# Optimization experiments

Measured on AMD Instinct MI355X. Metric: run time of the kernel, lower is better.

Reference implementation:

```python
import jax, jax.numpy as jnp
import numpy as np

EPS = 1e-12
B, S, H, NH = 4, 2048, 512, 8
DH = H // NH

def layernorm(x, g, b):
    mu = jnp.mean(x, axis=-1, keepdims=True)
    var = jnp.mean((x - mu) ** 2, axis=-1, keepdims=True)
    return (x - mu) * jax.lax.rsqrt(var + EPS) * g + b

def setup_inputs() -> dict:
    key = jax.random.key(0)
    ks = jax.random.split(key, 12)
    s = 0.02
    return {
        "hidden_states": jax.random.normal(ks[0], (B, S, H), dtype=jnp.float32),
        "attention_mask": jnp.zeros((B, 1, 1, S), dtype=jnp.float32),
        "ln1_g": jnp.ones((H,), jnp.float32), "ln1_b": jnp.zeros((H,), jnp.float32),
        "wq": jax.random.normal(ks[1], (H, H), jnp.float32) * s, "bq": jnp.zeros((H,), jnp.float32),
        "wk": jax.random.normal(ks[2], (H, H), jnp.float32) * s, "bk": jnp.zeros((H,), jnp.float32),
        "wv": jax.random.normal(ks[3], (H, H), jnp.float32) * s, "bv": jnp.zeros((H,), jnp.float32),
        "wo": jax.random.normal(ks[4], (H, H), jnp.float32) * s, "bo": jnp.zeros((H,), jnp.float32),
        "ln2_g": jnp.ones((H,), jnp.float32), "ln2_b": jnp.zeros((H,), jnp.float32),
    }

def _heads(x):  # [B,S,H] -> [B,NH,S,DH]
    return x.reshape(B, S, NH, DH).transpose(0, 2, 1, 3)

def reference(hidden_states, attention_mask, ln1_g, ln1_b, wq, bq, wk, bk, wv, bv, wo, bo, ln2_g, ln2_b):
    h = layernorm(hidden_states, ln1_g, ln1_b)  # Pre-LN
    q = _heads(h @ wq.T + bq)
    k = _heads(h @ wk.T + bk)
    v = _heads(h @ wv.T + bv)
    scores = jnp.einsum("bhqd,bhkd->bhqk", q, k) / jnp.sqrt(jnp.float32(DH))
    scores = scores + attention_mask  # additive BERT mask
    probs = jax.nn.softmax(scores, axis=-1)
    ctx = jnp.einsum("bhqk,bhkd->bhqd", probs, v)
    ctx = ctx.transpose(0, 2, 1, 3).reshape(B, S, H)
    # BertSelfOutput: LN(dense(ctx) + residual), residual is the LN'd hidden per module code
    out = layernorm(ctx @ wo.T + bo + h, ln2_g, ln2_b)
    return out
```

## Files before the change

### kernel.cpp

```cpp
#include <hip/hip_runtime.h>

typedef __bf16 bf16;
typedef __bf16 bf16x2 __attribute__((ext_vector_type(2)));
typedef __bf16 bf16x4 __attribute__((ext_vector_type(4)));
typedef __bf16 bf16x8 __attribute__((ext_vector_type(8)));
typedef float f32x4 __attribute__((ext_vector_type(4)));

typedef __attribute__((address_space(1))) const void g_void;
typedef __attribute__((address_space(3))) void l_void;

constexpr int Bsz = 4, S = 2048, H = 512, NH = 8, DH = 64;
constexpr int M = Bsz * S;
constexpr int K = H;
constexpr int WELEM = H * H;
constexpr float LOG2E  = 1.44269504f;
constexpr float QSCALE = 0.125f * LOG2E;

__global__ __launch_bounds__(256) void prep(
    const float* __restrict__ hidden, const float* __restrict__ ln1_g,
    const float* __restrict__ ln1_b,
    const float* __restrict__ w0, const float* __restrict__ w1,
    const float* __restrict__ w2, const float* __restrict__ w3,
    const float* __restrict__ mask,
    bf16* __restrict__ h, bf16* __restrict__ wb, float* __restrict__ mask2) {
    int bx = blockIdx.x;
    int t = threadIdx.x;
    if (bx < M) {
        int row = bx;
        float2 xv = *(const float2*)(hidden + (size_t)row * H + t * 2);
        float v0 = xv.x, v1 = xv.y;
        float s = v0 + v1, s2 = v0 * v0 + v1 * v1;
        for (int off = 1; off < 64; off <<= 1) {
            s  += __shfl_xor(s,  off, 64);
            s2 += __shfl_xor(s2, off, 64);
        }
        __shared__ float red[8];
        int wid = t >> 6;
        if ((t & 63) == 0) { red[wid * 2] = s; red[wid * 2 + 1] = s2; }
        __syncthreads();
        s  = red[0] + red[2] + red[4] + red[6];
        s2 = red[1] + red[3] + red[5] + red[7];
        float mu  = s * (1.0f / H);
        float var = s2 * (1.0f / H) - mu * mu;
        float inv = rsqrtf(var + 1e-12f);
        float2 gv = *(const float2*)(ln1_g + t * 2);
        float2 bv = *(const float2*)(ln1_b + t * 2);
        bf16x2 out;
        out.x = (bf16)((v0 - mu) * inv * gv.x + bv.x);
        out.y = (bf16)((v1 - mu) * inv * gv.y + bv.y);
        *(bf16x2*)(h + (size_t)row * H + t * 2) = out;
    } else if (bx < M + 1024) {
        int idx = bx - M;
        int y = idx >> 8, xx = idx & 255;
        const float* src = (y == 0) ? w0 : (y == 1) ? w1 : (y == 2) ? w2 : w3;
        bf16* d = wb + (size_t)y * WELEM;
        int i = (xx * 256 + t) * 4;
        float4 v = *(const float4*)(src + i);
        bf16x4 o;
        o.x = (bf16)v.x; o.y = (bf16)v.y; o.z = (bf16)v.z; o.w = (bf16)v.w;
        *(bf16x4*)(d + i) = o;
    } else {
        int i = (bx - M - 1024) * 256 + t;
        mask2[i] = mask[i] * LOG2E;
    }
}

__global__ __launch_bounds__(256) void ln_bf16_f32(
    const bf16* __restrict__ x, const float* __restrict__ g,
    const float* __restrict__ b, float* __restrict__ y) {
    int row = blockIdx.x;
    int t = threadIdx.x;
    bf16x2 xv = *(const bf16x2*)(x + (size_t)row * H + t * 2);
    float v0 = (float)xv.x, v1 = (float)xv.y;
    float s = v0 + v1, s2 = v0 * v0 + v1 * v1;
    for (int off = 1; off < 64; off <<= 1) {
        s  += __shfl_xor(s,  off, 64);
        s2 += __shfl_xor(s2, off, 64);
    }
    __shared__ float red[8];
    int wid = t >> 6;
    if ((t & 63) == 0) { red[wid * 2] = s; red[wid * 2 + 1] = s2; }
    __syncthreads();
    s  = red[0] + red[2] + red[4] + red[6];
    s2 = red[1] + red[3] + red[5] + red[7];
    float mu  = s * (1.0f / H);
    float var = s2 * (1.0f / H) - mu * mu;
    float inv = rsqrtf(var + 1e-12f);
    float2 gv = *(const float2*)(g + t * 2);
    float2 bv = *(const float2*)(b + t * 2);
    float2 out;
    out.x = (v0 - mu) * inv * gv.x + bv.x;
    out.y = (v1 - mu) * inv * gv.y + bv.y;
    *(float2*)(y + (size_t)row * H + t * 2) = out;
}

template<int BM, int BN, int MI, int NI>
__device__ inline void gemm_mainloop512(const bf16* __restrict__ A,
                                        const bf16* __restrict__ W,
                                        int bm, int bn,
                                        bf16* As, bf16* Bs, f32x4 acc[MI][NI]) {
    int t = threadIdx.x;
    int lane = t & 63, wid = t >> 6;
    int quad = lane >> 4, n = lane & 15;
    int wm = wid & 1, wn = wid >> 1;
    int sw = (n & 7) * 8;
    int srow = lane >> 3;
    int scol = (lane & 7) * 8;
    constexpr int APW = BM / 64;
    constexpr int BPW = BN / 64;
    constexpr int RM = MI * 16;
    constexpr int RN = NI * 16;
    for (int kt = 0; kt < K; kt += 64) {
        __syncthreads();
        #pragma unroll
        for (int i = 0; i < APW; i++) {
            int chunk = wid * APW + i;
            int row = chunk * 8 + srow;
            int csrc = scol ^ ((row & 7) * 8);
            __builtin_amdgcn_global_load_lds(
                (g_void*)&A[(size_t)(bm + row) * K + kt + csrc],
                (l_void*)&As[chunk * 512], 16, 0, 0);
        }
        #pragma unroll
        for (int i = 0; i < BPW; i++) {
            int chunk = wid * BPW + i;
            int row = chunk * 8 + srow;
            int csrc = scol ^ ((row & 7) * 8);
            __builtin_amdgcn_global_load_lds(
                (g_void*)&W[(size_t)(bn + row) * K + kt + csrc],
                (l_void*)&Bs[chunk * 512], 16, 0, 0);
        }
        __syncthreads();
        #pragma unroll
        for (int half = 0; half < 2; half++) {
            bf16x8 af[MI], bfr[NI];
            int c = (half * 32 + quad * 8) ^ sw;
            #pragma unroll
            for (int mi = 0; mi < MI; mi++)
                af[mi] = *(const bf16x8*)&As[(wm * RM + mi * 16 + n) * 64 + c];
            #pragma unroll
            for (int ni = 0; ni < NI; ni++)
                bfr[ni] = *(const bf16x8*)&Bs[(wn * RN + ni * 16 + n) * 64 + c];
            #pragma unroll
            for (int mi = 0; mi < MI; mi++)
                #pragma unroll
                for (int ni = 0; ni < NI; ni++)
                    acc[mi][ni] = __builtin_amdgcn_mfma_f32_16x16x32_bf16(
                        af[mi], bfr[ni], acc[mi][ni], 0, 0, 0);
        }
    }
}

__global__ __launch_bounds__(512, 4) void gemm_qkv(
    const bf16* __restrict__ h, const bf16* __restrict__ wb,
    const float* __restrict__ bq, const float* __restrict__ bk,
    const float* __restrict__ bv,
    bf16* __restrict__ qd, bf16* __restrict__ kd, bf16* __restrict__ vtd) {
    __shared__ alignas(16) bf16 smem[17408];
    bf16* As = smem;
    bf16* Bs = smem + 8192;
    int bm = blockIdx.x * 128, bn = blockIdx.y * 128, z = blockIdx.z;
    const bf16* W = wb + (size_t)z * WELEM;
    const float* bias = (z == 0) ? bq : (z == 1) ? bk : bv;
    f32x4 acc[4][2];
    for (int mi = 0; mi < 4; mi++)
        for (int ni = 0; ni < 2; ni++)
            for (int r = 0; r < 4; r++) acc[mi][ni][r] = 0.0f;
    gemm_mainloop512<128, 128, 4, 2>(h, W, bm, bn, As, Bs, acc);
    int t = threadIdx.x;
    int lane = t & 63, wid = t >> 6;
    int quad = lane >> 4, n = lane & 15;
    int wm = wid & 1, wn = wid >> 1;
    if (z < 2) {
        bf16* dst = (z == 0) ? qd : kd;
        for (int mi = 0; mi < 4; mi++)
            for (int ni = 0; ni < 2; ni++)
                for (int r = 0; r < 4; r++) {
                    int i = bm + wm * 64 + mi * 16 + quad * 4 + r;
                    int j = bn + wn * 32 + ni * 16 + n;
                    float val = acc[mi][ni][r] + bias[j];
                    if (z == 0) val *= QSCALE;
                    int b = i >> 11, srow = i & (S - 1);
                    int nh = j >> 6, d = j & (DH - 1);
                    dst[(((size_t)(b * NH + nh)) * S + srow) * DH + d] = (bf16)val;
                }
    } else {
        __syncthreads();
        bf16* T = smem;
        for (int mi = 0; mi < 4; mi++)
            for (int ni = 0; ni < 2; ni++)
                for (int r = 0; r < 4; r++) {
                    int il = wm * 64 + mi * 16 + quad * 4 + r;
                    int jl = wn * 32 + ni * 16 + n;
                    float val = acc[mi][ni][r] + bias[bn + jl];
                    T[jl * 136 + il] = (bf16)val;
                }
        __syncthreads();
        int b = bm >> 11, srow0 = bm & (S - 1);
        int c16 = t & 15;
        #pragma unroll
        for (int p = 0; p < 4; p++) {
            int jl = (t >> 4) + p * 32;
            int j = bn + jl;
            int nh = j >> 6, d = j & (DH - 1);
            bf16x8 v = *(const bf16x8*)&T[jl * 136 + c16 * 8];
            *(bf16x8*)&vtd[(((size_t)(b * NH + nh)) * DH + d) * S
                           + srow0 + c16 * 8] = v;
        }
    }
}

__global__ __launch_bounds__(512, 4) void gemm_out(
    const bf16* __restrict__ ctx, const bf16* __restrict__ wo,
    const float* __restrict__ bo, const bf16* __restrict__ resid,
    bf16* __restrict__ dst) {
    __shared__ alignas(16) bf16 As[64 * 64];
    __shared__ alignas(16) bf16 Bs[128 * 64];
    int bm = blockIdx.x * 64, bn = blockIdx.y * 128;
    f32x4 acc[2][2];
    for (int mi = 0; mi < 2; mi++)
        for (int ni = 0; ni < 2; ni++)
            for (int r = 0; r < 4; r++) acc[mi][ni][r] = 0.0f;
    gemm_mainloop512<64, 128, 2, 2>(ctx, wo, bm, bn, As, Bs, acc);
    int lane = threadIdx.x & 63, wid = threadIdx.x >> 6;
    int quad = lane >> 4, n = lane & 15;
    int wm = wid & 1, wn = wid >> 1;
    for (int mi = 0; mi < 2; mi++)
        for (int ni = 0; ni < 2; ni++)
            for (int r = 0; r < 4; r++) {
                int i = bm + wm * 32 + mi * 16 + quad * 4 + r;
                int j = bn + wn * 32 + ni * 16 + n;
                float val = acc[mi][ni][r] + bo[j]
                          + (float)resid[(size_t)i * H + j];
                dst[(size_t)i * H + j] = (bf16)val;
            }
}

constexpr int LDP9 = 72;

#if __has_builtin(__builtin_amdgcn_exp2f)
#define EXP2(x) __builtin_amdgcn_exp2f(x)
#else
#define EXP2(x) exp2f(x)
#endif

__global__ __launch_bounds__(512, 4) void attn_kernel(
    const bf16* __restrict__ q, const bf16* __restrict__ k,
    const bf16* __restrict__ vt, const float* __restrict__ mask2,
    bf16* __restrict__ ctx) {
    int bh = blockIdx.y;
    int b = bh >> 3, nh = bh & 7;
    int t = threadIdx.x, wid = t >> 6, lane = t & 63;
    int quad = lane >> 4, n = lane & 15;
    int qg = wid >> 1, kh = wid & 1;
    int qbase = blockIdx.x * 128 + qg * 32;
    int kO = kh * 64;

    const bf16* Qp = q  + (size_t)bh * S * DH;
    const bf16* Kp = k  + (size_t)bh * S * DH;
    const bf16* Vt = vt + (size_t)bh * DH * S;
    const float* mrow = mask2 + (size_t)b * S;

    __shared__ alignas(16) bf16 smem[34816];
    bf16* Ks = smem;
    bf16* Vs = smem + 8192;
    bf16* Pw = smem + 16384 + wid * (32 * LDP9);

    int sw = (n & 7) * 8;

    bf16x8 qf[2][2];
    #pragma unroll
    for (int qt = 0; qt < 2; qt++)
        #pragma unroll
        for (int hh = 0; hh < 2; hh++)
            qf[qt][hh] = *(const bf16x8*)
                &Qp[(size_t)(qbase + qt * 16 + n) * DH + hh * 32 + quad * 8];

    f32x4 O[2][4];
    #pragma unroll
    for (int qt = 0; qt < 2; qt++)
        for (int i = 0; i < 4; i++)
            for (int r = 0; r < 4; r++) O[qt][i][r] = 0.0f;
    float l_run[2] = {0.0f, 0.0f};

    for (int kb = 0; kb < S; kb += 128) {
        __syncthreads();
        #pragma unroll
        for (int i = 0; i < 2; i++) {
            int c = t + i * 512;
            {
                int row = c >> 3, part = c & 7;
                int csrc = (part * 8) ^ ((row & 7) * 8);
                __builtin_amdgcn_global_load_lds(
                    (g_void*)&Kp[(size_t)(kb + row) * DH + csrc],
                    (l_void*)&Ks[c * 8], 16, 0, 0);
            }
            {
                int row = c >> 4, part = c & 15;
                int csrc = (part * 8) ^ ((row & 7) * 8);
                __builtin_amdgcn_global_load_lds(
                    (g_void*)&Vt[(size_t)row * S + kb + csrc],
                    (l_void*)&Vs[c * 8], 16, 0, 0);
            }
        }
        __syncthreads();

        #pragma unroll
        for (int kt = 0; kt < 4; kt++) {
            const bf16* kr = &Ks[(kO + kt * 16 + n) * 64];
            bf16x8 ka = *(const bf16x8*)&kr[(quad * 8) ^ sw];
            bf16x8 kc = *(const bf16x8*)&kr[(32 + quad * 8) ^ sw];
            float4 mk = *(const float4*)&mrow[kb + kO + kt * 16 + quad * 4];
            #pragma unroll
            for (int qt = 0; qt < 2; qt++) {
                f32x4 s;
                for (int r = 0; r < 4; r++) s[r] = 0.0f;
                s = __builtin_amdgcn_mfma_f32_16x16x32_bf16(ka, qf[qt][0], s, 0, 0, 0);
                s = __builtin_amdgcn_mfma_f32_16x16x32_bf16(kc, qf[qt][1], s, 0, 0, 0);
                float p0 = EXP2(s[0] + mk.x);
                float p1 = EXP2(s[1] + mk.y);
                float p2 = EXP2(s[2] + mk.z);
                float p3 = EXP2(s[3] + mk.w);
                l_run[qt] += (p0 + p1) + (p2 + p3);
                bf16x4 w;
                w[0] = (bf16)p0; w[1] = (bf16)p1; w[2] = (bf16)p2; w[3] = (bf16)p3;
                *(bf16x4*)&Pw[(qt * 16 + n) * LDP9 + kt * 16 + quad * 4] = w;
            }
        }

        __builtin_amdgcn_s_setprio(1);
        #pragma unroll
        for (int ks = 0; ks < 2; ks++)
            #pragma unroll
            for (int qt = 0; qt < 2; qt++) {
                bf16x8 pf = *(const bf16x8*)
                    &Pw[(qt * 16 + n) * LDP9 + ks * 32 + quad * 8];
                #pragma unroll
                for (int dt = 0; dt < 4; dt++) {
                    bf16x8 vf = *(const bf16x8*)
                        &Vs[(dt * 16 + n) * 128 + ((kO + ks * 32 + quad * 8) ^ sw)];
                    O[qt][dt] = __builtin_amdgcn_mfma_f32_16x16x32_bf16(
                        vf, pf, O[qt][dt], 0, 0, 0);
                }
            }
        __builtin_amdgcn_s_setprio(0);
    }

    float* Ob = (float*)smem;
    float* Lb = Ob + 4 * 32 * 68;
    __syncthreads();
    if (kh) {
        #pragma unroll
        for (int qt = 0; qt < 2; qt++) {
            #pragma unroll
            for (int dt = 0; dt < 4; dt++)
                *(f32x4*)&Ob[(qg * 32 + qt * 16 + n) * 68 + dt * 16 + quad * 4]
                    = O[qt][dt];
            Lb[(qg * 2 + qt) * 64 + lane] = l_run[qt];
        }
    }
    __syncthreads();
    if (!kh) {
        #pragma unroll
        for (int qt = 0; qt < 2; qt++) {
            float l = l_run[qt] + Lb[(qg * 2 + qt) * 64 + lane];
            l += __shfl_xor(l, 16, 64);
            l += __shfl_xor(l, 32, 64);
            float linv = 1.0f / l;
            int srow = qbase + qt * 16 + n;
            #pragma unroll
            for (int dt = 0; dt < 4; dt++) {
                f32x4 po = *(const f32x4*)
                    &Ob[(qg * 32 + qt * 16 + n) * 68 + dt * 16 + quad * 4];
                bf16x4 o4;
                for (int r = 0; r < 4; r++)
                    o4[r] = (bf16)((O[qt][dt][r] + po[r]) * linv);
                int col = nh * 64 + dt * 16 + quad * 4;
                *(bf16x4*)&ctx[((size_t)(b * S + srow)) * H + col] = o4;
            }
        }
    }
}

extern "C" void kernel_launch(void* const* d_in, const int* in_sizes, int n_in,
                              void* d_out, int out_size, void* d_ws, size_t ws_size,
                              hipStream_t stream) {
    const float* hidden = (const float*)d_in[0];
    const float* mask   = (const float*)d_in[1];
    const float* ln1_g  = (const float*)d_in[2];
    const float* ln1_b  = (const float*)d_in[3];
    const float* wq = (const float*)d_in[4],  *bq = (const float*)d_in[5];
    const float* wk = (const float*)d_in[6],  *bk = (const float*)d_in[7];
    const float* wv = (const float*)d_in[8],  *bv = (const float*)d_in[9];
    const float* wo = (const float*)d_in[10], *bo = (const float*)d_in[11];
    const float* ln2_g = (const float*)d_in[12];
    const float* ln2_b = (const float*)d_in[13];

    const size_t T = (size_t)M * H;
    bf16* wb  = (bf16*)d_ws;
    bf16* h   = wb  + (size_t)4 * WELEM;
    bf16* qd  = h   + T;
    bf16* kd  = qd  + T;
    bf16* vtd = kd  + T;
    bf16* ctx = vtd + T;
    float* mask2 = (float*)(ctx + T);
    bf16* tmp = qd;

    prep<<<M + 1024 + 32, 256, 0, stream>>>(
        hidden, ln1_g, ln1_b, wq, wk, wv, wo, mask, h, wb, mask2);
    gemm_qkv<<<dim3(M / 128, H / 128, 3), 512, 0, stream>>>(
        h, wb, bq, bk, bv, qd, kd, vtd);
    attn_kernel<<<dim3(S / 128, Bsz * NH), 512, 0, stream>>>(qd, kd, vtd, mask2, ctx);
    gemm_out<<<dim3(M / 64, H / 128), 512, 0, stream>>>(
        ctx, wb + (size_t)3 * WELEM, bo, h, tmp);
    ln_bf16_f32<<<M, 256, 0, stream>>>(tmp, ln2_g, ln2_b, (float*)d_out);
}
```

Before: 178.4 us.

## Fuse LN2 into output GEMM via last-block counter; register-prefetch attention K/V tiles

```diff
diff --git a/kernel.cpp b/kernel.cpp
--- a/kernel.cpp
+++ b/kernel.cpp
@@ -22,7 +22,8 @@
     const float* __restrict__ w0, const float* __restrict__ w1,
     const float* __restrict__ w2, const float* __restrict__ w3,
     const float* __restrict__ mask,
-    bf16* __restrict__ h, bf16* __restrict__ wb, float* __restrict__ mask2) {
+    bf16* __restrict__ h, bf16* __restrict__ wb, float* __restrict__ mask2,
+    unsigned int* __restrict__ cnt) {
     int bx = blockIdx.x;
     int t = threadIdx.x;
     if (bx < M) {
@@ -59,39 +60,12 @@
         bf16x4 o;
         o.x = (bf16)v.x; o.y = (bf16)v.y; o.z = (bf16)v.z; o.w = (bf16)v.w;
         *(bf16x4*)(d + i) = o;
-    } else {
+    } else if (bx < M + 1024 + 32) {
         int i = (bx - M - 1024) * 256 + t;
         mask2[i] = mask[i] * LOG2E;
-    }
-}
-
-__global__ __launch_bounds__(256) void ln_bf16_f32(
-    const bf16* __restrict__ x, const float* __restrict__ g,
-    const float* __restrict__ b, float* __restrict__ y) {
-    int row = blockIdx.x;
-    int t = threadIdx.x;
-    bf16x2 xv = *(const bf16x2*)(x + (size_t)row * H + t * 2);
-    float v0 = (float)xv.x, v1 = (float)xv.y;
-    float s = v0 + v1, s2 = v0 * v0 + v1 * v1;
-    for (int off = 1; off < 64; off <<= 1) {
-        s  += __shfl_xor(s,  off, 64);
-        s2 += __shfl_xor(s2, off, 64);
-    }
-    __shared__ float red[8];
-    int wid = t >> 6;
-    if ((t & 63) == 0) { red[wid * 2] = s; red[wid * 2 + 1] = s2; }
-    __syncthreads();
-    s  = red[0] + red[2] + red[4] + red[6];
-    s2 = red[1] + red[3] + red[5] + red[7];
-    float mu  = s * (1.0f / H);
-    float var = s2 * (1.0f / H) - mu * mu;
-    float inv = rsqrtf(var + 1e-12f);
-    float2 gv = *(const float2*)(g + t * 2);
-    float2 bv = *(const float2*)(b + t * 2);
-    float2 out;
-    out.x = (v0 - mu) * inv * gv.x + bv.x;
-    out.y = (v1 - mu) * inv * gv.y + bv.y;
-    *(float2*)(y + (size_t)row * H + t * 2) = out;
+    } else {
+        if (t < 128) cnt[t] = 0u;
+    }
 }
 
 template<int BM, int BN, int MI, int NI>
@@ -210,19 +184,23 @@
     }
 }
 
-__global__ __launch_bounds__(512, 4) void gemm_out(
+__global__ __launch_bounds__(512, 4) void gemm_out_ln2(
     const bf16* __restrict__ ctx, const bf16* __restrict__ wo,
     const float* __restrict__ bo, const bf16* __restrict__ resid,
-    bf16* __restrict__ dst) {
+    const float* __restrict__ g2, const float* __restrict__ b2,
+    bf16* __restrict__ tmp, float* __restrict__ out,
+    unsigned int* __restrict__ cnt) {
     __shared__ alignas(16) bf16 As[64 * 64];
     __shared__ alignas(16) bf16 Bs[128 * 64];
+    __shared__ unsigned int lastFlag;
     int bm = blockIdx.x * 64, bn = blockIdx.y * 128;
     f32x4 acc[2][2];
     for (int mi = 0; mi < 2; mi++)
         for (int ni = 0; ni < 2; ni++)
             for (int r = 0; r < 4; r++) acc[mi][ni][r] = 0.0f;
     gemm_mainloop512<64, 128, 2, 2>(ctx, wo, bm, bn, As, Bs, acc);
-    int lane = threadIdx.x & 63, wid = threadIdx.x >> 6;
+    int t = threadIdx.x;
+    int lane = t & 63, wid = t >> 6;
     int quad = lane >> 4, n = lane & 15;
     int wm = wid & 1, wn = wid >> 1;
     for (int mi = 0; mi < 2; mi++)
@@ -232,8 +210,49 @@
                 int j = bn + wn * 32 + ni * 16 + n;
                 float val = acc[mi][ni][r] + bo[j]
                           + (float)resid[(size_t)i * H + j];
-                dst[(size_t)i * H + j] = (bf16)val;
-            }
+                tmp[(size_t)i * H + j] = (bf16)val;
+            }
+    __threadfence();
+    if (t == 0)
+        lastFlag = (atomicAdd(&cnt[blockIdx.x], 1u) == 3u) ? 1u : 0u;
+    __syncthreads();
+    if (lastFlag) {
+        __threadfence();
+        float4 ga = *(const float4*)&g2[lane * 8];
+        float4 gb = *(const float4*)&g2[lane * 8 + 4];
+        float4 ba = *(const float4*)&b2[lane * 8];
+        float4 bb = *(const float4*)&b2[lane * 8 + 4];
+        #pragma unroll
+        for (int rr = 0; rr < 8; rr++) {
+            int row = bm + rr * 8 + wid;
+            bf16x8 xv = *(const bf16x8*)&tmp[(size_t)row * H + lane * 8];
+            float v[8];
+            float s = 0.0f, s2 = 0.0f;
+            #pragma unroll
+            for (int e = 0; e < 8; e++) {
+                v[e] = (float)xv[e];
+                s += v[e]; s2 += v[e] * v[e];
+            }
+            for (int off = 1; off < 64; off <<= 1) {
+                s  += __shfl_xor(s,  off, 64);
+                s2 += __shfl_xor(s2, off, 64);
+            }
+            float mu  = s * (1.0f / H);
+            float var = s2 * (1.0f / H) - mu * mu;
+            float inv = rsqrtf(var + 1e-12f);
+            float4 o0, o1;
+            o0.x = (v[0] - mu) * inv * ga.x + ba.x;
+            o0.y = (v[1] - mu) * inv * ga.y + ba.y;
+            o0.z = (v[2] - mu) * inv * ga.z + ba.z;
+            o0.w = (v[3] - mu) * inv * ga.w + ba.w;
+            o1.x = (v[4] - mu) * inv * gb.x + bb.x;
+            o1.y = (v[5] - mu) * inv * gb.y + bb.y;
+            o1.z = (v[6] - mu) * inv * gb.z + bb.z;
+            o1.w = (v[7] - mu) * inv * gb.w + bb.w;
+            *(float4*)&out[(size_t)row * H + lane * 8]     = o0;
+            *(float4*)&out[(size_t)row * H + lane * 8 + 4] = o1;
+        }
+    }
 }
 
 constexpr int LDP9 = 72;
@@ -268,6 +287,14 @@
 
     int sw = (n & 7) * 8;
 
+    int krow = t >> 3;
+    int kcs  = ((t & 7) * 8) ^ ((krow & 7) * 8);
+    size_t koff = (size_t)krow * DH + kcs;
+    int vr0 = t >> 4,        vc0 = ((t & 15) * 8) ^ ((vr0 & 7) * 8);
+    int vr1 = (t + 512) >> 4, vc1 = ((t & 15) * 8) ^ ((vr1 & 7) * 8);
+    size_t voff0 = (size_t)vr0 * S + vc0;
+    size_t voff1 = (size_t)vr1 * S + vc1;
+
     bf16x8 qf[2][2];
     #pragma unroll
     for (int qt = 0; qt < 2; qt++)
@@ -283,27 +310,22 @@
             for (int r = 0; r < 4; r++) O[qt][i][r] = 0.0f;
     float l_run[2] = {0.0f, 0.0f};
 
+    uint4 kreg  = *(const uint4*)&Kp[koff];
+    uint4 vreg0 = *(const uint4*)&Vt[voff0];
+    uint4 vreg1 = *(const uint4*)&Vt[voff1];
+
     for (int kb = 0; kb < S; kb += 128) {
         __syncthreads();
-        #pragma unroll
-        for (int i = 0; i < 2; i++) {
-            int c = t + i * 512;
-            {
-                int row = c >> 3, part = c & 7;
-                int csrc = (part * 8) ^ ((row & 7) * 8);
-                __builtin_amdgcn_global_load_lds(
-                    (g_void*)&Kp[(size_t)(kb + row) * DH + csrc],
-                    (l_void*)&Ks[c * 8], 16, 0, 0);
-            }
-            {
-                int row = c >> 4, part = c & 15;
-                int csrc = (part * 8) ^ ((row & 7) * 8);
-                __builtin_amdgcn_global_load_lds(
-                    (g_void*)&Vt[(size_t)row * S + kb + csrc],
-                    (l_void*)&Vs[c * 8], 16, 0, 0);
-            }
-        }
-        __syncthreads();
+        *(uint4*)&Ks[(size_t)t * 8] = kreg;
+        *(uint4*)&Vs[(size_t)t * 8] = vreg0;
+        *(uint4*)&Vs[(size_t)(t + 512) * 8] = vreg1;
+        __syncthreads();
+
+        if (kb + 128 < S) {
+            kreg  = *(const uint4*)&Kp[koff + (size_t)(kb + 128) * DH];
+            vreg0 = *(const uint4*)&Vt[voff0 + (kb + 128)];
+            vreg1 = *(const uint4*)&Vt[voff1 + (kb + 128)];
+        }
 
         #pragma unroll
         for (int kt = 0; kt < 4; kt++) {
@@ -404,14 +426,15 @@
     bf16* vtd = kd  + T;
     bf16* ctx = vtd + T;
     float* mask2 = (float*)(ctx + T);
+    unsigned int* cnt = (unsigned int*)(mask2 + (size_t)Bsz * S);
     bf16* tmp = qd;
 
-    prep<<<M + 1024 + 32, 256, 0, stream>>>(
-        hidden, ln1_g, ln1_b, wq, wk, wv, wo, mask, h, wb, mask2);
+    prep<<<M + 1024 + 32 + 1, 256, 0, stream>>>(
+        hidden, ln1_g, ln1_b, wq, wk, wv, wo, mask, h, wb, mask2, cnt);
     gemm_qkv<<<dim3(M / 128, H / 128, 3), 512, 0, stream>>>(
         h, wb, bq, bk, bv, qd, kd, vtd);
     attn_kernel<<<dim3(S / 128, Bsz * NH), 512, 0, stream>>>(qd, kd, vtd, mask2, ctx);
-    gemm_out<<<dim3(M / 64, H / 128), 512, 0, stream>>>(
-        ctx, wb + (size_t)3 * WELEM, bo, h, tmp);
-    ln_bf16_f32<<<M, 256, 0, stream>>>(tmp, ln2_g, ln2_b, (float*)d_out);
-}
+    gemm_out_ln2<<<dim3(M / 64, H / 128), 512, 0, stream>>>(
+        ctx, wb + (size_t)3 * WELEM, bo, h, ln2_g, ln2_b, tmp,
+        (float*)d_out, cnt);
+}
```

After: 322.1 us. 80.6% more time.
